# Performance work log

Measured on AMD Instinct MI355X. Metric: run time of the kernel, lower is better.

## Reference

```python
import jax, jax.numpy as jnp
import numpy as np

D, T, B = 128, 64, 512
EPS = 1e-5


def setup_inputs() -> dict:
    key = jax.random.key(0)
    k1, k2, k3, k4, k5 = jax.random.split(key, 5)
    inp = jax.random.normal(k1, (D, T, B), jnp.float32) * 0.1
    returns_partition = jax.random.normal(k2, (D, T, B), jnp.float32) * 0.01
    target = jax.random.normal(k3, (D,), jnp.float32) * 0.1
    hidden = jnp.zeros((D, 1, B), jnp.float32)  # forward arg (overwritten at t=0)
    # diagonally-dominant weight so the per-row denominators v[j,j] stay away from 0
    W = jnp.eye(D, dtype=jnp.float32) + 0.1 * jax.random.normal(k4, (D, D), jnp.float32)
    b = 0.1 * jax.random.normal(k5, (D,), jnp.float32)
    return {"input": inp, "target": target, "returns_partition": returns_partition,
            "hidden": hidden, "W": W, "b": b}


def _recurrence(h, v, absb, pi_bar):
    # h, pi_bar: [D, B]; v: [D, D] (row-normalized); absb: [D]
    d = h.shape[0]
    vd = jnp.diagonal(v)                                  # v[j, j], torch.matmul(vj, e_j)
    s = v @ (h - pi_bar)                                  # [D, B], s[j] = vj . (h - pi_bar)
    lam_p = (absb[:, None] - s) / vd[:, None]
    lam_m = (-absb[:, None] - s) / vd[:, None]
    delta = (jnp.where(s > absb[:, None], lam_p, 0.0)
             + jnp.where(s < -absb[:, None], lam_m, 0.0))  # [D, B]
    # hidden_new_j = h + delta[j] * e_j  =>  v @ (hidden_new_j - pi_bar) = s + v[:, j] (x) delta[j]
    snew = s[None, :, :] + v.T[:, :, None] * delta[:, None, :]      # [J, D, B]
    inside = (snew < absb[None, :, None] + EPS) & (snew > -absb[None, :, None] - EPS)
    # torch: judge_mat[j] = min over rows; then max over j  == any_j(all_k(...))
    judge_mat = jnp.any(jnp.all(inside, axis=1), axis=0).astype(h.dtype)  # [B]

    # sequential per-coordinate projection (order matters: row j uses updated state)
    def body(ht, j):
        sj = v[j] @ (ht - pi_bar)                          # [B]
        lp = (absb[j] - sj) / v[j, j]
        lm = (-absb[j] - sj) / v[j, j]
        dj = jnp.where(sj > absb[j], lp, 0.0) + jnp.where(sj < -absb[j], lm, 0.0)
        return ht.at[j].add(dj), None
    h_temp, _ = jax.lax.scan(body, h, jnp.arange(d))

    # 10-step bisection between pi_bar (feasible) and (1 - judge_mat) * h
    def bis(carry, _):
        h_in, h_out = carry
        h_m = h_in + (h_out - h_in) * 0.5
        sm = v @ (h_m - pi_bar)
        j = jnp.all((sm <= absb[:, None] + EPS) & (sm >= -absb[:, None] - EPS), axis=0)  # [B]
        return (jnp.where(j, h_m, h_in), jnp.where(j, h_out, h_m)), h_m
    h_out0 = (1.0 - judge_mat) * h
    _, h_ms = jax.lax.scan(bis, (pi_bar, h_out0), None, length=10)
    h_m = h_ms[-1]
    return judge_mat * h_temp + (1.0 - judge_mat) * h_m


def reference(input, target, returns_partition, hidden, W, b):
    d, t, bsz = input.shape
    norm = jnp.linalg.norm(W, axis=1, keepdims=True)
    v = W / jnp.maximum(norm, 1e-12)                      # F.normalize(W, p=2, dim=1)
    absb = jnp.abs(b)
    pi_bar = jnp.broadcast_to(target[:, None], (d, bsz))  # [D, B]

    h0 = input[:, 0, :]                                   # t = 0: hidden := input slice
    rs = jnp.moveaxis(returns_partition[:, :t - 1, :], 1, 0)  # [T-1, D, B]

    def step(h, r):
        adj = h * (1.0 + r) / (1.0 + jnp.sum(h * r, axis=0))
        hn = _recurrence(adj, v, absb, pi_bar)
        return hn, hn

    h_last, hs = jax.lax.scan(step, h0, rs)
    output = jnp.concatenate([h0[:, None, :], jnp.moveaxis(hs, 0, 1)], axis=1)  # [D, T, B]
    return output, h_last[:, None, :]
```

## Files before the change

kernel.cpp:

```cpp
#include <hip/hip_runtime.h>
#include <cstdint>

#define D 128
#define T 64
#define B 512
#define EPSF 1e-5f

__device__ __forceinline__ float lane_bcast(float x, int l) {
    return __int_as_float(__builtin_amdgcn_readlane(__float_as_int(x), l));
}

__global__ __launch_bounds__(64) void prep_kernel(const float* __restrict__ W,
                                                  const float* __restrict__ b,
                                                  float* __restrict__ vT,
                                                  float* __restrict__ vd,
                                                  float* __restrict__ absb) {
    const int i = blockIdx.x;
    const int l = threadIdx.x;
    float w0 = W[i * D + l];
    float w1 = W[i * D + l + 64];
    float p = w0 * w0 + w1 * w1;
#pragma unroll
    for (int off = 32; off; off >>= 1) p += __shfl_xor(p, off);
    float norm = sqrtf(p);
    float scale = norm > 1e-12f ? norm : 1e-12f;
    float v0 = w0 / scale;
    float v1 = w1 / scale;
    vT[l * D + i] = v0;
    vT[(l + 64) * D + i] = v1;
    if (i < 64) {
        if (l == i) vd[i] = v0;
    } else {
        if (l == i - 64) vd[i] = v1;
    }
    if (i == 0) {
        absb[l] = fabsf(b[l]);
        absb[l + 64] = fabsf(b[l + 64]);
    }
}

__global__ __launch_bounds__(128, 1) void rnn_kernel(const float* __restrict__ input,
                                                     const float* __restrict__ target,
                                                     const float* __restrict__ returns,
                                                     const float* __restrict__ vTg,
                                                     const float* __restrict__ vdg,
                                                     const float* __restrict__ absbg,
                                                     float* __restrict__ out) {
    __shared__ float vsh[D * D];

    const int tid = threadIdx.x;
    {
        const float4* src = (const float4*)vTg;
        float4* dst = (float4*)vsh;
#pragma unroll
        for (int c = 0; c < 32; ++c) {
            int f = c * 128 + tid;
            int k = f >> 5;
            int i = (f & 31) << 2;
            int ck = (k & 7) << 2;
            int d4 = k * 32 + (((i ^ ck)) >> 2);
            dst[d4] = src[f];
        }
    }
    __syncthreads();

    const int w = tid >> 6;
    const int lane = tid & 63;
    const int b = blockIdx.x * 2 + w;
    const int rlo = lane, rhi = lane + 64;

    const float tgt_lo = target[rlo], tgt_hi = target[rhi];
    const float a_lo = absbg[rlo], a_hi = absbg[rhi];
    const float aeps_lo = a_lo + EPSF, aeps_hi = a_hi + EPSF;
    const float vd_lo = vdg[rlo], vd_hi = vdg[rhi];
    const float rvd_lo = 1.0f / vd_lo, rvd_hi = 1.0f / vd_hi;

    int ax[8];
#pragma unroll
    for (int c = 0; c < 8; ++c) ax[c] = rlo ^ (c << 2);

    float vl[D], vh[D];
#pragma unroll
    for (int k = 0; k < D; ++k) {
        int base = k * 128 + ax[k & 7];
        vl[k] = vsh[base];
        vh[k] = vsh[base + 64];
        asm volatile("" : "+a"(vl[k]), "+a"(vh[k]));
    }

    const int cj = (lane & 7) << 2;
    int Abase[8];
#pragma unroll
    for (int c = 0; c < 8; ++c) Abase[c] = lane * 128 + ((c << 2) ^ cj);

    float h_lo = input[rlo * T * B + b];
    float h_hi = input[rhi * T * B + b];
    out[rlo * T * B + b] = h_lo;
    out[rhi * T * B + b] = h_hi;

    float r_lo = returns[rlo * T * B + b];
    float r_hi = returns[rhi * T * B + b];

    for (int t = 1; t < T; ++t) {
        float num_lo = h_lo * (1.0f + r_lo);
        float num_hi = h_hi * (1.0f + r_hi);
        float p = h_lo * r_lo + h_hi * r_hi;
#pragma unroll
        for (int off = 32; off; off >>= 1) p += __shfl_xor(p, off);
        float den = 1.0f + p;
        float adj_lo = num_lo / den;
        float adj_hi = num_hi / den;

        if (t < T - 1) {
            r_lo = returns[rlo * T * B + t * B + b];
            r_hi = returns[rhi * T * B + t * B + b];
        }

        const float x_lo = adj_lo - tgt_lo;
        const float x_hi = adj_hi - tgt_hi;

        float s_lo = 0.0f, s_hi = 0.0f;
#pragma unroll
        for (int k = 0; k < 64; ++k) {
            float xb = lane_bcast(x_lo, k);
            s_lo = fmaf(vl[k], xb, s_lo);
            s_hi = fmaf(vh[k], xb, s_hi);
        }
#pragma unroll
        for (int k = 0; k < 64; ++k) {
            float xb = lane_bcast(x_hi, k);
            s_lo = fmaf(vl[64 + k], xb, s_lo);
            s_hi = fmaf(vh[64 + k], xb, s_hi);
        }

        h_lo = adj_lo;
        h_hi = adj_hi;

        bool viol_lo = (s_lo > a_lo) || (s_lo < -a_lo);
        bool viol_hi = (s_hi > a_hi) || (s_hi < -a_hi);
        uint64_t mlo = __ballot(viol_lo);
        uint64_t mhi = __ballot(viol_hi);

        if ((mlo | mhi) != 0ull) {
            float dl = 0.0f, dh = 0.0f;
            if (s_lo > a_lo) dl = (a_lo - s_lo) / vd_lo;
            else if (s_lo < -a_lo) dl = (-a_lo - s_lo) / vd_lo;
            if (s_hi > a_hi) dh = (a_hi - s_hi) / vd_hi;
            else if (s_hi < -a_hi) dh = (-a_hi - s_hi) / vd_hi;

            int V = __popcll(mlo) + __popcll(mhi);
            bool judge;

            if (V <= 8) {
                bool in_lo = (s_lo < aeps_lo) && (s_lo > -aeps_lo);
                bool in_hi = (s_hi < aeps_hi) && (s_hi > -aeps_hi);
                judge = (__ballot(in_lo && in_hi) == ~0ull);
                if (!judge) {
                    uint64_t t_mlo = mlo, t_mhi = mhi;
                    while (t_mlo | t_mhi) {
                        int j;
                        float dj;
                        if (t_mlo) {
                            int jl = (int)__ffsll((unsigned long long)t_mlo) - 1;
                            t_mlo &= t_mlo - 1;
                            j = jl;
                            dj = lane_bcast(dl, jl);
                        } else {
                            int jh = (int)__ffsll((unsigned long long)t_mhi) - 1;
                            t_mhi &= t_mhi - 1;
                            j = 64 + jh;
                            dj = lane_bcast(dh, jh);
                        }
                        int cjj = (j & 7) << 2;
                        int base = j * 128 + (rlo ^ cjj);
                        float n_lo = fmaf(vsh[base], dj, s_lo);
                        float n_hi = fmaf(vsh[base + 64], dj, s_hi);
                        bool pl = (n_lo < aeps_lo) && (n_lo > -aeps_lo);
                        bool ph = (n_hi < aeps_hi) && (n_hi > -aeps_hi);
                        if (__ballot(pl && ph) == ~0ull) { judge = true; break; }
                    }
                }
            } else {
                float m1 = -1.0f, m2 = -1.0f;
#pragma unroll
                for (int a = 0; a < 4; ++a) {
#pragma unroll
                    for (int c = 0; c < 8; ++c) {
                        const int i0 = a * 32 + c * 4;
                        const float* p1 = &vsh[Abase[c] + 32 * a];
                        float4 c1 = *(const float4*)p1;
                        float4 c2 = *(const float4*)(p1 + 8192);
#pragma unroll
                        for (int e = 0; e < 4; ++e) {
                            const int i = i0 + e;
                            float sv = (i < 64) ? lane_bcast(s_lo, i)
                                                : lane_bcast(s_hi, i - 64);
                            float ae = (i < 64) ? lane_bcast(aeps_lo, i)
                                                : lane_bcast(aeps_hi, i - 64);
                            float f1 = ((const float*)&c1)[e];
                            float f2 = ((const float*)&c2)[e];
                            m1 = fmaxf(m1, fabsf(fmaf(f1, dl, sv)) - ae);
                            m2 = fmaxf(m2, fabsf(fmaf(f2, dh, sv)) - ae);
                        }
                    }
                }
                judge = ((__ballot(m1 < 0.0f) | __ballot(m2 < 0.0f)) != 0ull);
            }

            if (judge) {
                uint64_t rem_lo = ~0ull, rem_hi = ~0ull;
                while (true) {
                    uint64_t m1b = __ballot((s_lo > a_lo) || (s_lo < -a_lo)) & rem_lo;
                    uint64_t m2b = __ballot((s_hi > a_hi) || (s_hi < -a_hi)) & rem_hi;
                    int j;
                    if (m1b) {
                        int jl = (int)__ffsll((unsigned long long)m1b) - 1;
                        j = jl;
                        rem_lo = (jl == 63) ? 0ull : (~0ull << (jl + 1));
                    } else if (m2b) {
                        int jh = (int)__ffsll((unsigned long long)m2b) - 1;
                        j = 64 + jh;
                        rem_lo = 0ull;
                        rem_hi = (jh == 63) ? 0ull : (~0ull << (jh + 1));
                    } else {
                        break;
                    }
                    float dl2 = (s_lo > a_lo) ? (a_lo - s_lo) * rvd_lo
                               : ((s_lo < -a_lo) ? (-a_lo - s_lo) * rvd_lo : 0.0f);
                    float dh2 = (s_hi > a_hi) ? (a_hi - s_hi) * rvd_hi
                               : ((s_hi < -a_hi) ? (-a_hi - s_hi) * rvd_hi : 0.0f);
                    float srcv = (j < 64) ? dl2 : dh2;
                    float dj = lane_bcast(srcv, j & 63);
                    if (lane == (j & 63)) {
                        if (j < 64) h_lo += dj; else h_hi += dj;
                    }
                    int cjj = (j & 7) << 2;
                    int base = j * 128 + (rlo ^ cjj);
                    s_lo = fmaf(vsh[base], dj, s_lo);
                    s_hi = fmaf(vsh[base + 64], dj, s_hi);
                }
            } else {
                float hin_lo = tgt_lo, hin_hi = tgt_hi;
                float sin_lo = 0.0f, sin_hi = 0.0f;
                float hout_lo = h_lo, hout_hi = h_hi;
                float sout_lo = s_lo, sout_hi = s_hi;
                float hm_lo = 0.0f, hm_hi = 0.0f;
#pragma unroll
                for (int it = 0; it < 10; ++it) {
                    hm_lo = hin_lo + (hout_lo - hin_lo) * 0.5f;
                    hm_hi = hin_hi + (hout_hi - hin_hi) * 0.5f;
                    float sm_lo = sin_lo + (sout_lo - sin_lo) * 0.5f;
                    float sm_hi = sin_hi + (sout_hi - sin_hi) * 0.5f;
                    bool pl = (sm_lo <= aeps_lo) && (sm_lo >= -aeps_lo);
                    bool ph = (sm_hi <= aeps_hi) && (sm_hi >= -aeps_hi);
                    bool inside = (__ballot(pl && ph) == ~0ull);
                    if (inside) {
                        hin_lo = hm_lo; hin_hi = hm_hi;
                        sin_lo = sm_lo; sin_hi = sm_hi;
                    } else {
                        hout_lo = hm_lo; hout_hi = hm_hi;
                        sout_lo = sm_lo; sout_hi = sm_hi;
                    }
                }
                h_lo = hm_lo;
                h_hi = hm_hi;
            }
        }

        out[rlo * T * B + t * B + b] = h_lo;
        out[rhi * T * B + t * B + b] = h_hi;
    }

    out[D * T * B + rlo * B + b] = h_lo;
    out[D * T * B + rhi * B + b] = h_hi;
}

extern "C" void kernel_launch(void* const* d_in, const int* in_sizes, int n_in,
                              void* d_out, int out_size, void* d_ws, size_t ws_size,
                              hipStream_t stream) {
    const float* input   = (const float*)d_in[0];
    const float* target  = (const float*)d_in[1];
    const float* returns = (const float*)d_in[2];
    const float* W = (const float*)d_in[4];
    const float* b = (const float*)d_in[5];
    float* out = (float*)d_out;

    float* vT   = (float*)d_ws;
    float* vd   = vT + D * D;
    float* absb = vd + D;

    prep_kernel<<<D, 64, 0, stream>>>(W, b, vT, vd, absb);
    rnn_kernel<<<B / 2, 128, 0, stream>>>(input, target, returns, vT, vd, absb, out);
}
```

Before: 215.8 us.

## Transpose returns/input/output to batch-major layout for coalesced access in RNN kernel

Adds tiled shared-memory transpose kernels that convert returns and the t=0 input into a [T,B,D]-style layout in workspace. The recurrent kernel then reads and writes contiguous per-batch rows, and a final transpose writes the output back in the original layout, including the h_last slice. The aim is to replace strided per-timestep global accesses with coalesced ones, at the cost of extra kernel launches and full-tensor copies through memory. If the workspace is too small it falls back to the old strided path.

```diff
diff --git a/kernel.cpp b/kernel.cpp
--- a/kernel.cpp
+++ b/kernel.cpp
@@ -39,13 +39,64 @@
     }
 }
 
+__global__ __launch_bounds__(256) void transpose_in(const float* __restrict__ src,
+                                                    float* __restrict__ dst) {
+    __shared__ float tile[64][65];
+    const int TBc = T * B;
+    const int c0 = blockIdx.x * 64;
+    const int r0 = blockIdx.y * 64;
+    const int lx = threadIdx.x & 63;
+    const int ly = threadIdx.x >> 6;
+#pragma unroll
+    for (int i = 0; i < 16; ++i) {
+        int rr = ly + i * 4;
+        tile[rr][lx] = src[(r0 + rr) * TBc + c0 + lx];
+    }
+    __syncthreads();
+#pragma unroll
+    for (int i = 0; i < 16; ++i) {
+        int cc = ly + i * 4;
+        dst[(c0 + cc) * D + r0 + lx] = tile[lx][cc];
+    }
+}
+
+__global__ __launch_bounds__(256) void transpose_out_k(const float* __restrict__ src,
+                                                       float* __restrict__ dst) {
+    __shared__ float tile[64][65];
+    const int TBc = T * B;
+    const int c0 = blockIdx.x * 64;
+    const int r0 = blockIdx.y * 64;
+    const int lx = threadIdx.x & 63;
+    const int ly = threadIdx.x >> 6;
+#pragma unroll
+    for (int i = 0; i < 16; ++i) {
+        int cc = ly + i * 4;
+        tile[cc][lx] = src[(c0 + cc) * D + r0 + lx];
+    }
+    __syncthreads();
+#pragma unroll
+    for (int i = 0; i < 16; ++i) {
+        int rr = ly + i * 4;
+        dst[(r0 + rr) * TBc + c0 + lx] = tile[lx][rr];
+    }
+    if (c0 >= (T - 1) * B) {
+        const int boff = c0 - (T - 1) * B;
+#pragma unroll
+        for (int i = 0; i < 16; ++i) {
+            int rr = ly + i * 4;
+            dst[D * TBc + (r0 + rr) * B + boff + lx] = tile[lx][rr];
+        }
+    }
+}
+
+template <int COAL>
 __global__ __launch_bounds__(128, 1) void rnn_kernel(const float* __restrict__ input,
                                                      const float* __restrict__ target,
-                                                     const float* __restrict__ returns,
+                                                     const float* __restrict__ rets,
                                                      const float* __restrict__ vTg,
                                                      const float* __restrict__ vdg,
                                                      const float* __restrict__ absbg,
-                                                     float* __restrict__ out) {
+                                                     float* __restrict__ outp) {
     __shared__ float vsh[D * D];
 
     const int tid = threadIdx.x;
@@ -93,13 +144,22 @@
 #pragma unroll
     for (int c = 0; c < 8; ++c) Abase[c] = lane * 128 + ((c << 2) ^ cj);
 
-    float h_lo = input[rlo * T * B + b];
-    float h_hi = input[rhi * T * B + b];
-    out[rlo * T * B + b] = h_lo;
-    out[rhi * T * B + b] = h_hi;
-
-    float r_lo = returns[rlo * T * B + b];
-    float r_hi = returns[rhi * T * B + b];
+    float h_lo, h_hi, r_lo, r_hi;
+    if (COAL) {
+        h_lo = input[(b << 7) + rlo];
+        h_hi = input[(b << 7) + rhi];
+        outp[(b << 7) + rlo] = h_lo;
+        outp[(b << 7) + rhi] = h_hi;
+        r_lo = rets[(b << 7) + rlo];
+        r_hi = rets[(b << 7) + rhi];
+    } else {
+        h_lo = input[rlo * T * B + b];
+        h_hi = input[rhi * T * B + b];
+        outp[rlo * T * B + b] = h_lo;
+        outp[rhi * T * B + b] = h_hi;
+        r_lo = rets[rlo * T * B + b];
+        r_hi = rets[rhi * T * B + b];
+    }
 
     for (int t = 1; t < T; ++t) {
         float num_lo = h_lo * (1.0f + r_lo);
@@ -112,8 +172,13 @@
         float adj_hi = num_hi / den;
 
         if (t < T - 1) {
-            r_lo = returns[rlo * T * B + t * B + b];
-            r_hi = returns[rhi * T * B + t * B + b];
+            if (COAL) {
+                r_lo = rets[((t * B + b) << 7) + rlo];
+                r_hi = rets[((t * B + b) << 7) + rhi];
+            } else {
+                r_lo = rets[rlo * T * B + t * B + b];
+                r_hi = rets[rhi * T * B + t * B + b];
+            }
         }
 
         const float x_lo = adj_lo - tgt_lo;
@@ -267,12 +332,19 @@
             }
         }
 
-        out[rlo * T * B + t * B + b] = h_lo;
-        out[rhi * T * B + t * B + b] = h_hi;
-    }
-
-    out[D * T * B + rlo * B + b] = h_lo;
-    out[D * T * B + rhi * B + b] = h_hi;
+        if (COAL) {
+            outp[((t * B + b) << 7) + rlo] = h_lo;
+            outp[((t * B + b) << 7) + rhi] = h_hi;
+        } else {
+            outp[rlo * T * B + t * B + b] = h_lo;
+            outp[rhi * T * B + t * B + b] = h_hi;
+        }
+    }
+
+    if (!COAL) {
+        outp[D * T * B + rlo * B + b] = h_lo;
+        outp[D * T * B + rhi * B + b] = h_hi;
+    }
 }
 
 extern "C" void kernel_launch(void* const* d_in, const int* in_sizes, int n_in,
@@ -288,7 +360,23 @@
     float* vT   = (float*)d_ws;
     float* vd   = vT + D * D;
     float* absb = vd + D;
+    float* inp0 = absb + D;
+    float* rett = inp0 + D * B;
+    float* outt = rett + (size_t)T * B * D;
+
+    const size_t need = ((size_t)(D * D + 2 * D + D * B) + 2ull * T * B * D)
+                        * sizeof(float);
 
     prep_kernel<<<D, 64, 0, stream>>>(W, b, vT, vd, absb);
-    rnn_kernel<<<B / 2, 128, 0, stream>>>(input, target, returns, vT, vd, absb, out);
-}
+
+    if (ws_size >= need) {
+        transpose_in<<<dim3(T * B / 64, 2), 256, 0, stream>>>(returns, rett);
+        transpose_in<<<dim3(B / 64, 2), 256, 0, stream>>>(input, inp0);
+        rnn_kernel<1><<<B / 2, 128, 0, stream>>>(inp0, target, rett, vT, vd,
+                                                 absb, outt);
+        transpose_out_k<<<dim3(T * B / 64, 2), 256, 0, stream>>>(outt, out);
+    } else {
+        rnn_kernel<0><<<B / 2, 128, 0, stream>>>(input, target, returns, vT,
+                                                 vd, absb, out);
+    }
+}
```

New measurement: 225.2 us. 4.4% more time.

## Process two batch columns per wavefront to reuse register-resident weights

Applied to the files above, without the earlier changes.

Each wavefront now carries two batch columns instead of one, sharing the register-held normalized weight matrix across both matvecs and interleaving their FMA chains. The grid is halved to B/4 blocks, and the correction logic is factored into a helper called once per column. This is meant to amortize the per-block weight load from shared memory into registers and to add instruction-level parallelism that hides readlane/FMA latency. The trade-off is fewer blocks (128 on a GPU with more CUs than that, so some CUs sit idle), higher register pressure, and serialized divergent correction paths for the two columns.

```diff
diff --git a/kernel.cpp b/kernel.cpp
--- a/kernel.cpp
+++ b/kernel.cpp
@@ -39,6 +39,147 @@
     }
 }
 
+__device__ __forceinline__ void correct_column(
+    float& h_lo, float& h_hi, float s_lo, float s_hi,
+    const float a_lo, const float a_hi,
+    const float aeps_lo, const float aeps_hi,
+    const float vd_lo, const float vd_hi,
+    const float rvd_lo, const float rvd_hi,
+    const float tgt_lo, const float tgt_hi,
+    const float* __restrict__ vsh, const int* Abase,
+    const int rlo, const int lane)
+{
+    bool viol_lo = (s_lo > a_lo) || (s_lo < -a_lo);
+    bool viol_hi = (s_hi > a_hi) || (s_hi < -a_hi);
+    uint64_t mlo = __ballot(viol_lo);
+    uint64_t mhi = __ballot(viol_hi);
+    if ((mlo | mhi) == 0ull) return;
+
+    float dl = 0.0f, dh = 0.0f;
+    if (s_lo > a_lo) dl = (a_lo - s_lo) / vd_lo;
+    else if (s_lo < -a_lo) dl = (-a_lo - s_lo) / vd_lo;
+    if (s_hi > a_hi) dh = (a_hi - s_hi) / vd_hi;
+    else if (s_hi < -a_hi) dh = (-a_hi - s_hi) / vd_hi;
+
+    int V = __popcll(mlo) + __popcll(mhi);
+    bool judge;
+
+    if (V <= 8) {
+        bool in_lo = (s_lo < aeps_lo) && (s_lo > -aeps_lo);
+        bool in_hi = (s_hi < aeps_hi) && (s_hi > -aeps_hi);
+        judge = (__ballot(in_lo && in_hi) == ~0ull);
+        if (!judge) {
+            uint64_t t_mlo = mlo, t_mhi = mhi;
+            while (t_mlo | t_mhi) {
+                int j;
+                float dj;
+                if (t_mlo) {
+                    int jl = (int)__ffsll((unsigned long long)t_mlo) - 1;
+                    t_mlo &= t_mlo - 1;
+                    j = jl;
+                    dj = lane_bcast(dl, jl);
+                } else {
+                    int jh = (int)__ffsll((unsigned long long)t_mhi) - 1;
+                    t_mhi &= t_mhi - 1;
+                    j = 64 + jh;
+                    dj = lane_bcast(dh, jh);
+                }
+                int cjj = (j & 7) << 2;
+                int base = j * 128 + (rlo ^ cjj);
+                float n_lo = fmaf(vsh[base], dj, s_lo);
+                float n_hi = fmaf(vsh[base + 64], dj, s_hi);
+                bool pl = (n_lo < aeps_lo) && (n_lo > -aeps_lo);
+                bool ph = (n_hi < aeps_hi) && (n_hi > -aeps_hi);
+                if (__ballot(pl && ph) == ~0ull) { judge = true; break; }
+            }
+        }
+    } else {
+        float m1 = -1.0f, m2 = -1.0f;
+#pragma unroll
+        for (int a = 0; a < 4; ++a) {
+#pragma unroll
+            for (int c = 0; c < 8; ++c) {
+                const int i0 = a * 32 + c * 4;
+                const float* p1 = &vsh[Abase[c] + 32 * a];
+                float4 c1 = *(const float4*)p1;
+                float4 c2 = *(const float4*)(p1 + 8192);
+#pragma unroll
+                for (int e = 0; e < 4; ++e) {
+                    const int i = i0 + e;
+                    float sv = (i < 64) ? lane_bcast(s_lo, i)
+                                        : lane_bcast(s_hi, i - 64);
+                    float ae = (i < 64) ? lane_bcast(aeps_lo, i)
+                                        : lane_bcast(aeps_hi, i - 64);
+                    float f1 = ((const float*)&c1)[e];
+                    float f2 = ((const float*)&c2)[e];
+                    m1 = fmaxf(m1, fabsf(fmaf(f1, dl, sv)) - ae);
+                    m2 = fmaxf(m2, fabsf(fmaf(f2, dh, sv)) - ae);
+                }
+            }
+        }
+        judge = ((__ballot(m1 < 0.0f) | __ballot(m2 < 0.0f)) != 0ull);
+    }
+
+    if (judge) {
+        uint64_t rem_lo = ~0ull, rem_hi = ~0ull;
+        while (true) {
+            uint64_t m1b = __ballot((s_lo > a_lo) || (s_lo < -a_lo)) & rem_lo;
+            uint64_t m2b = __ballot((s_hi > a_hi) || (s_hi < -a_hi)) & rem_hi;
+            int j;
+            if (m1b) {
+                int jl = (int)__ffsll((unsigned long long)m1b) - 1;
+                j = jl;
+                rem_lo = (jl == 63) ? 0ull : (~0ull << (jl + 1));
+            } else if (m2b) {
+                int jh = (int)__ffsll((unsigned long long)m2b) - 1;
+                j = 64 + jh;
+                rem_lo = 0ull;
+                rem_hi = (jh == 63) ? 0ull : (~0ull << (jh + 1));
+            } else {
+                break;
+            }
+            float dl2 = (s_lo > a_lo) ? (a_lo - s_lo) * rvd_lo
+                       : ((s_lo < -a_lo) ? (-a_lo - s_lo) * rvd_lo : 0.0f);
+            float dh2 = (s_hi > a_hi) ? (a_hi - s_hi) * rvd_hi
+                       : ((s_hi < -a_hi) ? (-a_hi - s_hi) * rvd_hi : 0.0f);
+            float srcv = (j < 64) ? dl2 : dh2;
+            float dj = lane_bcast(srcv, j & 63);
+            if (lane == (j & 63)) {
+                if (j < 64) h_lo += dj; else h_hi += dj;
+            }
+            int cjj = (j & 7) << 2;
+            int base = j * 128 + (rlo ^ cjj);
+            s_lo = fmaf(vsh[base], dj, s_lo);
+            s_hi = fmaf(vsh[base + 64], dj, s_hi);
+        }
+    } else {
+        float hin_lo = tgt_lo, hin_hi = tgt_hi;
+        float sin_lo = 0.0f, sin_hi = 0.0f;
+        float hout_lo = h_lo, hout_hi = h_hi;
+        float sout_lo = s_lo, sout_hi = s_hi;
+        float hm_lo = 0.0f, hm_hi = 0.0f;
+#pragma unroll
+        for (int it = 0; it < 10; ++it) {
+            hm_lo = hin_lo + (hout_lo - hin_lo) * 0.5f;
+            hm_hi = hin_hi + (hout_hi - hin_hi) * 0.5f;
+            float sm_lo = sin_lo + (sout_lo - sin_lo) * 0.5f;
+            float sm_hi = sin_hi + (sout_hi - sin_hi) * 0.5f;
+            bool pl = (sm_lo <= aeps_lo) && (sm_lo >= -aeps_lo);
+            bool ph = (sm_hi <= aeps_hi) && (sm_hi >= -aeps_hi);
+            bool inside = (__ballot(pl && ph) == ~0ull);
+            if (inside) {
+                hin_lo = hm_lo; hin_hi = hm_hi;
+                sin_lo = sm_lo; sin_hi = sm_hi;
+            } else {
+                hout_lo = hm_lo; hout_hi = hm_hi;
+                sout_lo = sm_lo; sout_hi = sm_hi;
+            }
+        }
+        h_lo = hm_lo;
+        h_hi = hm_hi;
+    }
+}
+
 __global__ __launch_bounds__(128, 1) void rnn_kernel(const float* __restrict__ input,
                                                      const float* __restrict__ target,
                                                      const float* __restrict__ returns,
@@ -66,7 +207,8 @@
 
     const int w = tid >> 6;
     const int lane = tid & 63;
-    const int b = blockIdx.x * 2 + w;
+    const int bA = blockIdx.x * 4 + w * 2;
+    const int bB = bA + 1;
     const int rlo = lane, rhi = lane + 64;
 
     const float tgt_lo = target[rlo], tgt_hi = target[rhi];
@@ -93,186 +235,93 @@
 #pragma unroll
     for (int c = 0; c < 8; ++c) Abase[c] = lane * 128 + ((c << 2) ^ cj);
 
-    float h_lo = input[rlo * T * B + b];
-    float h_hi = input[rhi * T * B + b];
-    out[rlo * T * B + b] = h_lo;
-    out[rhi * T * B + b] = h_hi;
-
-    float r_lo = returns[rlo * T * B + b];
-    float r_hi = returns[rhi * T * B + b];
+    float hA_lo = input[rlo * T * B + bA];
+    float hA_hi = input[rhi * T * B + bA];
+    float hB_lo = input[rlo * T * B + bB];
+    float hB_hi = input[rhi * T * B + bB];
+    out[rlo * T * B + bA] = hA_lo;
+    out[rhi * T * B + bA] = hA_hi;
+    out[rlo * T * B + bB] = hB_lo;
+    out[rhi * T * B + bB] = hB_hi;
+
+    float rA_lo = returns[rlo * T * B + bA];
+    float rA_hi = returns[rhi * T * B + bA];
+    float rB_lo = returns[rlo * T * B + bB];
+    float rB_hi = returns[rhi * T * B + bB];
 
     for (int t = 1; t < T; ++t) {
-        float num_lo = h_lo * (1.0f + r_lo);
-        float num_hi = h_hi * (1.0f + r_hi);
-        float p = h_lo * r_lo + h_hi * r_hi;
-#pragma unroll
-        for (int off = 32; off; off >>= 1) p += __shfl_xor(p, off);
-        float den = 1.0f + p;
-        float adj_lo = num_lo / den;
-        float adj_hi = num_hi / den;
+        float numA_lo = hA_lo * (1.0f + rA_lo);
+        float numA_hi = hA_hi * (1.0f + rA_hi);
+        float numB_lo = hB_lo * (1.0f + rB_lo);
+        float numB_hi = hB_hi * (1.0f + rB_hi);
+        float pA = hA_lo * rA_lo + hA_hi * rA_hi;
+        float pB = hB_lo * rB_lo + hB_hi * rB_hi;
+#pragma unroll
+        for (int off = 32; off; off >>= 1) {
+            pA += __shfl_xor(pA, off);
+            pB += __shfl_xor(pB, off);
+        }
+        float denA = 1.0f + pA;
+        float denB = 1.0f + pB;
+        float adjA_lo = numA_lo / denA;
+        float adjA_hi = numA_hi / denA;
+        float adjB_lo = numB_lo / denB;
+        float adjB_hi = numB_hi / denB;
 
         if (t < T - 1) {
-            r_lo = returns[rlo * T * B + t * B + b];
-            r_hi = returns[rhi * T * B + t * B + b];
-        }
-
-        const float x_lo = adj_lo - tgt_lo;
-        const float x_hi = adj_hi - tgt_hi;
-
-        float s_lo = 0.0f, s_hi = 0.0f;
+            rA_lo = returns[rlo * T * B + t * B + bA];
+            rA_hi = returns[rhi * T * B + t * B + bA];
+            rB_lo = returns[rlo * T * B + t * B + bB];
+            rB_hi = returns[rhi * T * B + t * B + bB];
+        }
+
+        const float xA_lo = adjA_lo - tgt_lo;
+        const float xA_hi = adjA_hi - tgt_hi;
+        const float xB_lo = adjB_lo - tgt_lo;
+        const float xB_hi = adjB_hi - tgt_hi;
+
+        float sA_lo = 0.0f, sA_hi = 0.0f, sB_lo = 0.0f, sB_hi = 0.0f;
 #pragma unroll
         for (int k = 0; k < 64; ++k) {
-            float xb = lane_bcast(x_lo, k);
-            s_lo = fmaf(vl[k], xb, s_lo);
-            s_hi = fmaf(vh[k], xb, s_hi);
+            float xa = lane_bcast(xA_lo, k);
+            float xb = lane_bcast(xB_lo, k);
+            sA_lo = fmaf(vl[k], xa, sA_lo);
+            sB_lo = fmaf(vl[k], xb, sB_lo);
+            sA_hi = fmaf(vh[k], xa, sA_hi);
+            sB_hi = fmaf(vh[k], xb, sB_hi);
         }
 #pragma unroll
         for (int k = 0; k < 64; ++k) {
-            float xb = lane_bcast(x_hi, k);
-            s_lo = fmaf(vl[64 + k], xb, s_lo);
-            s_hi = fmaf(vh[64 + k], xb, s_hi);
-        }
-
-        h_lo = adj_lo;
-        h_hi = adj_hi;
-
-        bool viol_lo = (s_lo > a_lo) || (s_lo < -a_lo);
-        bool viol_hi = (s_hi > a_hi) || (s_hi < -a_hi);
-        uint64_t mlo = __ballot(viol_lo);
-        uint64_t mhi = __ballot(viol_hi);
-
-        if ((mlo | mhi) != 0ull) {
-            float dl = 0.0f, dh = 0.0f;
-            if (s_lo > a_lo) dl = (a_lo - s_lo) / vd_lo;
-            else if (s_lo < -a_lo) dl = (-a_lo - s_lo) / vd_lo;
-            if (s_hi > a_hi) dh = (a_hi - s_hi) / vd_hi;
-            else if (s_hi < -a_hi) dh = (-a_hi - s_hi) / vd_hi;
-
-            int V = __popcll(mlo) + __popcll(mhi);
-            bool judge;
-
-            if (V <= 8) {
-                bool in_lo = (s_lo < aeps_lo) && (s_lo > -aeps_lo);
-                bool in_hi = (s_hi < aeps_hi) && (s_hi > -aeps_hi);
-                judge = (__ballot(in_lo && in_hi) == ~0ull);
-                if (!judge) {
-                    uint64_t t_mlo = mlo, t_mhi = mhi;
-                    while (t_mlo | t_mhi) {
-                        int j;
-                        float dj;
-                        if (t_mlo) {
-                            int jl = (int)__ffsll((unsigned long long)t_mlo) - 1;
-                            t_mlo &= t_mlo - 1;
-                            j = jl;
-                            dj = lane_bcast(dl, jl);
-                        } else {
-                            int jh = (int)__ffsll((unsigned long long)t_mhi) - 1;
-                            t_mhi &= t_mhi - 1;
-                            j = 64 + jh;
-                            dj = lane_bcast(dh, jh);
-                        }
-                        int cjj = (j & 7) << 2;
-                        int base = j * 128 + (rlo ^ cjj);
-                        float n_lo = fmaf(vsh[base], dj, s_lo);
-                        float n_hi = fmaf(vsh[base + 64], dj, s_hi);
-                        bool pl = (n_lo < aeps_lo) && (n_lo > -aeps_lo);
-                        bool ph = (n_hi < aeps_hi) && (n_hi > -aeps_hi);
-                        if (__ballot(pl && ph) == ~0ull) { judge = true; break; }
-                    }
-                }
-            } else {
-                float m1 = -1.0f, m2 = -1.0f;
-#pragma unroll
-                for (int a = 0; a < 4; ++a) {
-#pragma unroll
-                    for (int c = 0; c < 8; ++c) {
-                        const int i0 = a * 32 + c * 4;
-                        const float* p1 = &vsh[Abase[c] + 32 * a];
-                        float4 c1 = *(const float4*)p1;
-                        float4 c2 = *(const float4*)(p1 + 8192);
-#pragma unroll
-                        for (int e = 0; e < 4; ++e) {
-                            const int i = i0 + e;
-                            float sv = (i < 64) ? lane_bcast(s_lo, i)
-                                                : lane_bcast(s_hi, i - 64);
-                            float ae = (i < 64) ? lane_bcast(aeps_lo, i)
-                                                : lane_bcast(aeps_hi, i - 64);
-                            float f1 = ((const float*)&c1)[e];
-                            float f2 = ((const float*)&c2)[e];
-                            m1 = fmaxf(m1, fabsf(fmaf(f1, dl, sv)) - ae);
-                            m2 = fmaxf(m2, fabsf(fmaf(f2, dh, sv)) - ae);
-                        }
-                    }
-                }
-                judge = ((__ballot(m1 < 0.0f) | __ballot(m2 < 0.0f)) != 0ull);
-            }
-
-            if (judge) {
-                uint64_t rem_lo = ~0ull, rem_hi = ~0ull;
-                while (true) {
-                    uint64_t m1b = __ballot((s_lo > a_lo) || (s_lo < -a_lo)) & rem_lo;
-                    uint64_t m2b = __ballot((s_hi > a_hi) || (s_hi < -a_hi)) & rem_hi;
-                    int j;
-                    if (m1b) {
-                        int jl = (int)__ffsll((unsigned long long)m1b) - 1;
-                        j = jl;
-                        rem_lo = (jl == 63) ? 0ull : (~0ull << (jl + 1));
-                    } else if (m2b) {
-                        int jh = (int)__ffsll((unsigned long long)m2b) - 1;
-                        j = 64 + jh;
-                        rem_lo = 0ull;
-                        rem_hi = (jh == 63) ? 0ull : (~0ull << (jh + 1));
-                    } else {
-                        break;
-                    }
-                    float dl2 = (s_lo > a_lo) ? (a_lo - s_lo) * rvd_lo
-                               : ((s_lo < -a_lo) ? (-a_lo - s_lo) * rvd_lo : 0.0f);
-                    float dh2 = (s_hi > a_hi) ? (a_hi - s_hi) * rvd_hi
-                               : ((s_hi < -a_hi) ? (-a_hi - s_hi) * rvd_hi : 0.0f);
-                    float srcv = (j < 64) ? dl2 : dh2;
-                    float dj = lane_bcast(srcv, j & 63);
-                    if (lane == (j & 63)) {
-                        if (j < 64) h_lo += dj; else h_hi += dj;
-                    }
-                    int cjj = (j & 7) << 2;
-                    int base = j * 128 + (rlo ^ cjj);
-                    s_lo = fmaf(vsh[base], dj, s_lo);
-                    s_hi = fmaf(vsh[base + 64], dj, s_hi);
-                }
-            } else {
-                float hin_lo = tgt_lo, hin_hi = tgt_hi;
-                float sin_lo = 0.0f, sin_hi = 0.0f;
-                float hout_lo = h_lo, hout_hi = h_hi;
-                float sout_lo = s_lo, sout_hi = s_hi;
-                float hm_lo = 0.0f, hm_hi = 0.0f;
-#pragma unroll
-                for (int it = 0; it < 10; ++it) {
-                    hm_lo = hin_lo + (hout_lo - hin_lo) * 0.5f;
-                    hm_hi = hin_hi + (hout_hi - hin_hi) * 0.5f;
-                    float sm_lo = sin_lo + (sout_lo - sin_lo) * 0.5f;
-                    float sm_hi = sin_hi + (sout_hi - sin_hi) * 0.5f;
-                    bool pl = (sm_lo <= aeps_lo) && (sm_lo >= -aeps_lo);
-                    bool ph = (sm_hi <= aeps_hi) && (sm_hi >= -aeps_hi);
-                    bool inside = (__ballot(pl && ph) == ~0ull);
-                    if (inside) {
-                        hin_lo = hm_lo; hin_hi = hm_hi;
-                        sin_lo = sm_lo; sin_hi = sm_hi;
-                    } else {
-                        hout_lo = hm_lo; hout_hi = hm_hi;
-                        sout_lo = sm_lo; sout_hi = sm_hi;
-                    }
-                }
-                h_lo = hm_lo;
-                h_hi = hm_hi;
-            }
-        }
-
-        out[rlo * T * B + t * B + b] = h_lo;
-        out[rhi * T * B + t * B + b] = h_hi;
-    }
-
-    out[D * T * B + rlo * B + b] = h_lo;
-    out[D * T * B + rhi * B + b] = h_hi;
+            float xa = lane_bcast(xA_hi, k);
+            float xb = lane_bcast(xB_hi, k);
+            sA_lo = fmaf(vl[64 + k], xa, sA_lo);
+            sB_lo = fmaf(vl[64 + k], xb, sB_lo);
+            sA_hi = fmaf(vh[64 + k], xa, sA_hi);
+            sB_hi = fmaf(vh[64 + k], xb, sB_hi);
+        }
+
+        hA_lo = adjA_lo;
+        hA_hi = adjA_hi;
+        hB_lo = adjB_lo;
+        hB_hi = adjB_hi;
+
+        correct_column(hA_lo, hA_hi, sA_lo, sA_hi,
+                       a_lo, a_hi, aeps_lo, aeps_hi, vd_lo, vd_hi,
+                       rvd_lo, rvd_hi, tgt_lo, tgt_hi, vsh, Abase, rlo, lane);
+        correct_column(hB_lo, hB_hi, sB_lo, sB_hi,
+                       a_lo, a_hi, aeps_lo, aeps_hi, vd_lo, vd_hi,
+                       rvd_lo, rvd_hi, tgt_lo, tgt_hi, vsh, Abase, rlo, lane);
+
+        out[rlo * T * B + t * B + bA] = hA_lo;
+        out[rhi * T * B + t * B + bA] = hA_hi;
+        out[rlo * T * B + t * B + bB] = hB_lo;
+        out[rhi * T * B + t * B + bB] = hB_hi;
+    }
+
+    out[D * T * B + rlo * B + bA] = hA_lo;
+    out[D * T * B + rhi * B + bA] = hA_hi;
+    out[D * T * B + rlo * B + bB] = hB_lo;
+    out[D * T * B + rhi * B + bB] = hB_hi;
 }
 
 extern "C" void kernel_launch(void* const* d_in, const int* in_sizes, int n_in,
@@ -290,5 +339,5 @@
     float* absb = vd + D;
 
     prep_kernel<<<D, 64, 0, stream>>>(W, b, vT, vd, absb);
-    rnn_kernel<<<B / 2, 128, 0, stream>>>(input, target, returns, vT, vd, absb, out);
-}
+    rnn_kernel<<<B / 4, 128, 0, stream>>>(input, target, returns, vT, vd, absb, out);
+}
```

New measurement: 417.2 us. +93.3%, slower.
